# Kernel tuning notes

Hardware: AMD Instinct MI355X
Metric: run time of the kernel (lower is better)

Reference implementation:

```python
import jax, jax.numpy as jnp
import numpy as np
import math

B, S, H, NH = 8, 2048, 128, 4
DH = H // NH
SQRT_2_OVER_PI = math.sqrt(2.0 / math.pi)


def layer_norm(x, a, b, eps=1e-6):
    # Faithful to the torch module: unbiased std (ddof=1) and divide by (std + eps)
    mean = jnp.mean(x, axis=-1, keepdims=True)
    std = jnp.std(x, axis=-1, keepdims=True, ddof=1)
    return a * (x - mean) / (std + eps) + b


def setup_inputs() -> dict:
    key = jax.random.key(0)
    ks = jax.random.split(key, 10)
    inp = {
        "hidden": jax.random.normal(ks[0], (B, S, H), dtype=jnp.float32),
        "mask": jax.random.randint(ks[1], (B, S), 0, 2, dtype=jnp.int32),
        # attention params
        "attn_scale_w": jax.random.normal(ks[2], (NH, S), dtype=jnp.float32) * 0.1,
        "Wl": jax.random.normal(ks[3], (H, H), dtype=jnp.float32) * (1.0 / math.sqrt(H)),
        "bl": jnp.zeros((H,), dtype=jnp.float32),
        # FFN params
        "W1": jax.random.normal(ks[4], (H, H), dtype=jnp.float32) * (1.0 / math.sqrt(H)),
        "b1": jnp.zeros((H,), dtype=jnp.float32),
        "ffn_scale_w": jax.random.normal(ks[5], (S, 1), dtype=jnp.float32) * 0.1,
        # layer norms
        "ln1_a": jnp.ones((H,), dtype=jnp.float32),
        "ln1_b": jnp.zeros((H,), dtype=jnp.float32),
        "ln2_a": jnp.ones((H,), dtype=jnp.float32),
        "ln2_b": jnp.zeros((H,), dtype=jnp.float32),
    }
    return inp


def reference(hidden, mask, attn_scale_w, Wl, bl, W1, b1, ffn_scale_w,
              ln1_a, ln1_b, ln2_a, ln2_b):
    x = hidden  # [B, S, H]

    # --- attention sublayer (pre-norm residual) ---
    n1 = layer_norm(x, ln1_a, ln1_b)
    qkv = n1.reshape(B, S, NH, DH).transpose(0, 2, 1, 3)  # [B, NH, S, DH]
    # scores with per-head/per-query-position learned scale
    corr = jnp.einsum("bhqd,bhkd->bhqk", qkv, qkv) / math.sqrt(DH)
    corr = corr * attn_scale_w[None, :, :, None]  # scale over query positions
    # mask over key positions: [B,1,1,S], broadcast matches repeat in torch
    corr = jnp.where(mask[:, None, None, :] == 0, -1e9, corr)
    prob = jax.nn.softmax(corr, axis=-1)
    h = jnp.einsum("bhqk,bhkd->bhqd", prob, qkv)
    h = h.transpose(0, 2, 1, 3).reshape(B, S, H)
    attn_out = h @ Wl.T + bl
    x = x + attn_out

    # --- FFN sublayer (pre-norm residual) ---
    n2 = layer_norm(x, ln2_a, ln2_b)
    hf = ffn_scale_w[None] * (n2 @ W1.T + b1)  # [B, S, H] with per-position scale
    act = 0.5 * hf * (1.0 + jnp.tanh(SQRT_2_OVER_PI * (hf + 0.044715 * hf ** 3)))
    x = x + act

    return x
```

## Files before the change

### kernel.cpp

```cpp
#include <hip/hip_runtime.h>

#define BB 8
#define SS 2048
#define HH 128
#define NHH 4
#define DHH 32

typedef _Float16 f16;
typedef f16 f16x4 __attribute__((ext_vector_type(4)));
typedef f16 f16x8 __attribute__((ext_vector_type(8)));
typedef float f32x4 __attribute__((ext_vector_type(4)));

#define BIAS0 -5.7707801636f

__device__ __forceinline__ f16x8 cat(f16x4 a, f16x4 b) {
  return (f16x8){a[0], a[1], a[2], a[3], b[0], b[1], b[2], b[3]};
}

__device__ __forceinline__ f16x4 tr_read(const f16* p) {
  f16x4 d;
  asm volatile("ds_read_b64_tr_b16 %0, %1"
               : "=v"(d)
               : "v"((__attribute__((address_space(3))) const f16*)p)
               : "memory");
  return d;
}

__global__ __launch_bounds__(256) void stage1_kernel(const float* __restrict__ x,
                                                     const float* __restrict__ ga,
                                                     const float* __restrict__ gb,
                                                     const float* __restrict__ Wl,
                                                     const float* __restrict__ W1,
                                                     const int* __restrict__ mask,
                                                     f16* __restrict__ n1,
                                                     f16* __restrict__ Wlf,
                                                     f16* __restrict__ W1f,
                                                     int* __restrict__ idx,
                                                     int* __restrict__ nkcnt,
                                                     int* __restrict__ nkpad) {
  const int tid = threadIdx.x;
  if (blockIdx.x < 1024) {
    const int wave = tid >> 6, lane = tid & 63;
    const int grp = lane >> 4, lm = lane & 15;
    const int r = wave * 4 + grp;
    const size_t row = (size_t)blockIdx.x * 16 + r;

    const float* xr = x + row * HH + lm * 8;
    float4 v0 = *(const float4*)(xr);
    float4 v1 = *(const float4*)(xr + 4);
    float xv[8] = {v0.x, v0.y, v0.z, v0.w, v1.x, v1.y, v1.z, v1.w};
    float sum = 0.f, sq = 0.f;
#pragma unroll
    for (int j = 0; j < 8; ++j) { sum += xv[j]; sq += xv[j] * xv[j]; }
#pragma unroll
    for (int m = 1; m < 16; m <<= 1) {
      sum += __shfl_xor(sum, m);
      sq += __shfl_xor(sq, m);
    }
    float mean = sum * (1.0f / HH);
    float var = fmaxf((sq - (float)HH * mean * mean) * (1.0f / (HH - 1)), 0.0f);
    float inv = 1.0f / (sqrtf(var) + 1e-6f);

    float4 a0 = *(const float4*)(ga + lm * 8);
    float4 a1 = *(const float4*)(ga + lm * 8 + 4);
    float4 b0 = *(const float4*)(gb + lm * 8);
    float4 b1 = *(const float4*)(gb + lm * 8 + 4);
    float av[8] = {a0.x, a0.y, a0.z, a0.w, a1.x, a1.y, a1.z, a1.w};
    float bv[8] = {b0.x, b0.y, b0.z, b0.w, b1.x, b1.y, b1.z, b1.w};
    f16x8 w;
#pragma unroll
    for (int j = 0; j < 8; ++j) w[j] = (f16)(av[j] * (xv[j] - mean) * inv + bv[j]);
    *(f16x8*)(n1 + row * HH + lm * 8) = w;
    return;
  }
  if (blockIdx.x < 1056) {
    int g = (blockIdx.x - 1024) * 256 + tid;
    if (g < 4096) {
      float4 w = ((const float4*)Wl)[g];
      f16x4 o = {(f16)w.x, (f16)w.y, (f16)w.z, (f16)w.w};
      ((f16x4*)Wlf)[g] = o;
    } else {
      float4 w = ((const float4*)W1)[g - 4096];
      f16x4 o = {(f16)w.x, (f16)w.y, (f16)w.z, (f16)w.w};
      ((f16x4*)W1f)[g - 4096] = o;
    }
    return;
  }
  const int b = blockIdx.x - 1056;
  __shared__ int ps[256];
  int m8[8];
  int cnt = 0;
  const int* mp = mask + b * SS + tid * 8;
#pragma unroll
  for (int j = 0; j < 8; ++j) {
    m8[j] = mp[j];
    cnt += (m8[j] != 0);
  }
  ps[tid] = cnt;
  __syncthreads();
  for (int off = 1; off < 256; off <<= 1) {
    int v = (tid >= off) ? ps[tid - off] : 0;
    __syncthreads();
    ps[tid] += v;
    __syncthreads();
  }
  int pos = ps[tid] - cnt;
#pragma unroll
  for (int j = 0; j < 8; ++j) {
    if (m8[j] != 0) idx[b * SS + pos++] = tid * 8 + j;
  }
  __syncthreads();
  int nkv = ps[255];
  int npv = (nkv + 63) & ~63;
  if (npv == 0) npv = 64;
  for (int jj = nkv + tid; jj < npv; jj += 256) idx[b * SS + jj] = 0;
  if (tid == 255) { nkcnt[b] = nkv; nkpad[b] = npv; }
}

__global__ __launch_bounds__(256, 1) void attn_kernel(const f16* __restrict__ n1,
                                                      const int* __restrict__ idx,
                                                      const int* __restrict__ nkcnt,
                                                      const int* __restrict__ nkpad,
                                                      const float* __restrict__ scalew,
                                                      f16* __restrict__ hatt) {
  const int tid = threadIdx.x;
  const int qb = blockIdx.x & 7;
  const int h = (blockIdx.x >> 3) & 3;
  const int b = blockIdx.x >> 5;
  const int wave = tid >> 6, lane = tid & 63;
  const int lg = lane >> 4, lm = lane & 15;
  const int nk = nkcnt[b];
  const int ns = nkpad[b] >> 6;

  __shared__ __align__(16) f16 Kt[2][2][64][16];
  __shared__ __align__(16) int idxL[SS];

  const f16* __restrict__ nb = n1 + (size_t)b * SS * HH + h * DHH;

  const int np = ns << 6;
  for (int j = tid * 4; j < np; j += 1024)
    *(int4*)&idxL[j] = *(const int4*)(idx + b * SS + j);

  const int q0 = qb * 256 + wave * 64 + lm;
  f16x8 qf[4];
  float sc2[4];
#pragma unroll
  for (int qt = 0; qt < 4; ++qt) {
    int q = q0 + qt * 16;
    qf[qt] = *(const f16x8*)(nb + (size_t)q * HH + lg * 8);
    sc2[qt] = scalew[h * SS + q] * 0.2550680718664f;
  }

  const int sk = tid >> 2, sp = tid & 3;

  const f32x4 zero = {0.f, 0.f, 0.f, 0.f};
  f32x4 acc[4][2] = {{zero, zero}, {zero, zero}, {zero, zero}, {zero, zero}};
  f32x4 lacc[4] = {zero, zero, zero, zero};
  const f16x8 ones = {(f16)1, (f16)1, (f16)1, (f16)1, (f16)1, (f16)1, (f16)1, (f16)1};

  __syncthreads();
  {
    int row = idxL[sk];
    f16x8 kreg = *(const f16x8*)(nb + (size_t)row * HH + sp * 8);
    *(f16x8*)(&Kt[0][sp >> 1][sk][(sp & 1) * 8]) = kreg;
  }
  __syncthreads();

  for (int c = 0; c < ns; ++c) {
    const int buf = c & 1;
    const int k0 = c * 64;
    f16x8 kreg;
    if (c + 1 < ns) {
      int row = idxL[k0 + 64 + sk];
      kreg = *(const f16x8*)(nb + (size_t)row * HH + sp * 8);
    }
    f16x4 t0a = tr_read(&Kt[buf][0][0][0] + lane * 4);
    f16x4 t0b = tr_read(&Kt[buf][0][16][0] + lane * 4);
    f16x4 t0c = tr_read(&Kt[buf][0][32][0] + lane * 4);
    f16x4 t0d = tr_read(&Kt[buf][0][48][0] + lane * 4);
    f16x4 t1a = tr_read(&Kt[buf][1][0][0] + lane * 4);
    f16x4 t1b = tr_read(&Kt[buf][1][16][0] + lane * 4);
    f16x4 t1c = tr_read(&Kt[buf][1][32][0] + lane * 4);
    f16x4 t1d = tr_read(&Kt[buf][1][48][0] + lane * 4);

    f16x8 kf[4];
#pragma unroll
    for (int t = 0; t < 4; ++t)
      kf[t] = *(const f16x8*)(&Kt[buf][lg >> 1][t * 16 + lm][(lg & 1) * 8]);

    const bool tail = (k0 + 64 > nk);
    f16x8 pf[4][2];
#define PF_LOOP(MASKED)                                                                   \
  _Pragma("unroll") for (int qt = 0; qt < 4; ++qt) {                                      \
    _Pragma("unroll") for (int t = 0; t < 4; ++t) {                                       \
      f32x4 st = __builtin_amdgcn_mfma_f32_16x16x32_f16(kf[t], qf[qt], zero, 0, 0, 0);    \
      _Pragma("unroll") for (int r = 0; r < 4; ++r) {                                     \
        float pe = __builtin_amdgcn_exp2f(st[r] * sc2[qt] + BIAS0);                       \
        if (MASKED && (k0 + t * 16 + lg * 4 + r >= nk)) pe = 0.0f;                        \
        pf[qt][t >> 1][(t & 1) * 4 + r] = (f16)pe;                                        \
      }                                                                                   \
    }                                                                                     \
  }
    if (!tail) { PF_LOOP(false) } else { PF_LOOP(true) }
#undef PF_LOOP

#pragma unroll
    for (int qt = 0; qt < 4; ++qt) {
#pragma unroll
      for (int s = 0; s < 2; ++s)
        lacc[qt] = __builtin_amdgcn_mfma_f32_16x16x32_f16(ones, pf[qt][s], lacc[qt], 0, 0, 0);
    }

    asm volatile("s_waitcnt lgkmcnt(0)" ::: "memory");
    __builtin_amdgcn_sched_barrier(0);

    f16x8 vf;
    vf = cat(t0a, t0b);
#pragma unroll
    for (int qt = 0; qt < 4; ++qt)
      acc[qt][0] = __builtin_amdgcn_mfma_f32_16x16x32_f16(vf, pf[qt][0], acc[qt][0], 0, 0, 0);
    vf = cat(t1a, t1b);
#pragma unroll
    for (int qt = 0; qt < 4; ++qt)
      acc[qt][1] = __builtin_amdgcn_mfma_f32_16x16x32_f16(vf, pf[qt][0], acc[qt][1], 0, 0, 0);
    vf = cat(t0c, t0d);
#pragma unroll
    for (int qt = 0; qt < 4; ++qt)
      acc[qt][0] = __builtin_amdgcn_mfma_f32_16x16x32_f16(vf, pf[qt][1], acc[qt][0], 0, 0, 0);
    vf = cat(t1c, t1d);
#pragma unroll
    for (int qt = 0; qt < 4; ++qt)
      acc[qt][1] = __builtin_amdgcn_mfma_f32_16x16x32_f16(vf, pf[qt][1], acc[qt][1], 0, 0, 0);

    if (c + 1 < ns)
      *(f16x8*)(&Kt[buf ^ 1][sp >> 1][sk][(sp & 1) * 8]) = kreg;
    __syncthreads();
  }

#pragma unroll
  for (int qt = 0; qt < 4; ++qt) {
    float inv = 1.0f / lacc[qt][0];
    int q = q0 + qt * 16;
    f16* op = hatt + (size_t)(b * SS + q) * HH + h * DHH;
    f16x4 o0 = {(f16)(acc[qt][0][0] * inv), (f16)(acc[qt][0][1] * inv),
                (f16)(acc[qt][0][2] * inv), (f16)(acc[qt][0][3] * inv)};
    f16x4 o1 = {(f16)(acc[qt][1][0] * inv), (f16)(acc[qt][1][1] * inv),
                (f16)(acc[qt][1][2] * inv), (f16)(acc[qt][1][3] * inv)};
    *(f16x4*)(op + lg * 4) = o0;
    *(f16x4*)(op + 16 + lg * 4) = o1;
  }
}

__global__ __launch_bounds__(256) void mlp_kernel(const f16* __restrict__ X,
                                                  const f16* __restrict__ Wlf,
                                                  const float* __restrict__ bl,
                                                  const float* __restrict__ resid,
                                                  const float* __restrict__ ln2a,
                                                  const float* __restrict__ ln2b,
                                                  const f16* __restrict__ W1f,
                                                  const float* __restrict__ b1,
                                                  const float* __restrict__ fscale,
                                                  float* __restrict__ out) {
  const int tid = threadIdx.x;
  const int wave = tid >> 6, lane = tid & 63;
  const int lg = lane >> 4, lm = lane & 15;
  const int rbase = blockIdx.x * 32;
  const int nc0 = wave * 32;

  __shared__ __align__(16) f16 n2t[32][136];
  __shared__ float red[4][32][2];

  f32x4 acc[2][2] = {};
  const f16* xr0 = X + (size_t)(rbase + lm) * HH;
  const f16* xr1 = X + (size_t)(rbase + 16 + lm) * HH;
#pragma unroll
  for (int ks = 0; ks < 4; ++ks) {
    f16x8 bf0 = *(const f16x8*)(xr0 + ks * 32 + lg * 8);
    f16x8 bf1 = *(const f16x8*)(xr1 + ks * 32 + lg * 8);
#pragma unroll
    for (int nt = 0; nt < 2; ++nt) {
      f16x8 af = *(const f16x8*)(Wlf + (size_t)(nc0 + nt * 16 + lm) * HH + ks * 32 + lg * 8);
      acc[0][nt] = __builtin_amdgcn_mfma_f32_16x16x32_f16(af, bf0, acc[0][nt], 0, 0, 0);
      acc[1][nt] = __builtin_amdgcn_mfma_f32_16x16x32_f16(af, bf1, acc[1][nt], 0, 0, 0);
    }
  }
  float sum[2] = {0.f, 0.f}, sq[2] = {0.f, 0.f};
  f32x4 o[2][2];
#pragma unroll
  for (int g = 0; g < 2; ++g) {
    int row = rbase + g * 16 + lm;
#pragma unroll
    for (int nt = 0; nt < 2; ++nt) {
      int n = nc0 + nt * 16 + lg * 4;
      float4 rv = *(const float4*)(resid + (size_t)row * HH + n);
      float4 bv = *(const float4*)(bl + n);
      f32x4 v = acc[g][nt];
      v[0] += rv.x + bv.x; v[1] += rv.y + bv.y;
      v[2] += rv.z + bv.z; v[3] += rv.w + bv.w;
      o[g][nt] = v;
      sum[g] += v[0] + v[1] + v[2] + v[3];
      sq[g] += v[0] * v[0] + v[1] * v[1] + v[2] * v[2] + v[3] * v[3];
    }
    sum[g] += __shfl_xor(sum[g], 16); sum[g] += __shfl_xor(sum[g], 32);
    sq[g] += __shfl_xor(sq[g], 16);  sq[g] += __shfl_xor(sq[g], 32);
  }
  if (lane < 16) {
#pragma unroll
    for (int g = 0; g < 2; ++g) {
      red[wave][g * 16 + lm][0] = sum[g];
      red[wave][g * 16 + lm][1] = sq[g];
    }
  }
  __syncthreads();
#pragma unroll
  for (int g = 0; g < 2; ++g) {
    int lr = g * 16 + lm;
    float ts = red[0][lr][0] + red[1][lr][0] + red[2][lr][0] + red[3][lr][0];
    float tq = red[0][lr][1] + red[1][lr][1] + red[2][lr][1] + red[3][lr][1];
    float mean = ts * (1.0f / HH);
    float var = fmaxf((tq - (float)HH * mean * mean) * (1.0f / (HH - 1)), 0.0f);
    float inv = 1.0f / (sqrtf(var) + 1e-6f);
#pragma unroll
    for (int nt = 0; nt < 2; ++nt) {
      int n = nc0 + nt * 16 + lg * 4;
      float4 av = *(const float4*)(ln2a + n);
      float4 b2 = *(const float4*)(ln2b + n);
      f16x4 w;
      w[0] = (f16)(av.x * (o[g][nt][0] - mean) * inv + b2.x);
      w[1] = (f16)(av.y * (o[g][nt][1] - mean) * inv + b2.y);
      w[2] = (f16)(av.z * (o[g][nt][2] - mean) * inv + b2.z);
      w[3] = (f16)(av.w * (o[g][nt][3] - mean) * inv + b2.w);
      *(f16x4*)(&n2t[lr][n]) = w;
    }
  }
  __syncthreads();

  f32x4 fa[2][2] = {};
#pragma unroll
  for (int ks = 0; ks < 4; ++ks) {
    f16x8 bf0 = *(const f16x8*)(&n2t[lm][ks * 32 + lg * 8]);
    f16x8 bf1 = *(const f16x8*)(&n2t[16 + lm][ks * 32 + lg * 8]);
#pragma unroll
    for (int nt = 0; nt < 2; ++nt) {
      f16x8 af = *(const f16x8*)(W1f + (size_t)(nc0 + nt * 16 + lm) * HH + ks * 32 + lg * 8);
      fa[0][nt] = __builtin_amdgcn_mfma_f32_16x16x32_f16(af, bf0, fa[0][nt], 0, 0, 0);
      fa[1][nt] = __builtin_amdgcn_mfma_f32_16x16x32_f16(af, bf1, fa[1][nt], 0, 0, 0);
    }
  }
#pragma unroll
  for (int g = 0; g < 2; ++g) {
    int row = rbase + g * 16 + lm;
    float fs = fscale[row & (SS - 1)];
#pragma unroll
    for (int nt = 0; nt < 2; ++nt) {
      int n = nc0 + nt * 16 + lg * 4;
      float4 bv = *(const float4*)(b1 + n);
      const float* bp = &bv.x;
#pragma unroll
      for (int e = 0; e < 4; ++e) {
        float hf = fs * (fa[g][nt][e] + bp[e]);
        float u = 0.7978845608028654f * hf * (1.0f + 0.044715f * hf * hf);
        float ex = __builtin_amdgcn_exp2f(u * 2.8853900817779268f);
        float t = 1.0f - 2.0f / (ex + 1.0f);
        o[g][nt][e] += 0.5f * hf * (1.0f + t);
      }
      *(f32x4*)(out + (size_t)row * HH + n) = o[g][nt];
    }
  }
}

extern "C" void kernel_launch(void* const* d_in, const int* in_sizes, int n_in,
                              void* d_out, int out_size, void* d_ws, size_t ws_size,
                              hipStream_t stream) {
  const float* hidden = (const float*)d_in[0];
  const int* mask = (const int*)d_in[1];
  const float* scalew = (const float*)d_in[2];
  const float* Wl = (const float*)d_in[3];
  const float* bl = (const float*)d_in[4];
  const float* W1 = (const float*)d_in[5];
  const float* b1 = (const float*)d_in[6];
  const float* fscale = (const float*)d_in[7];
  const float* ln1a = (const float*)d_in[8];
  const float* ln1b = (const float*)d_in[9];
  const float* ln2a = (const float*)d_in[10];
  const float* ln2b = (const float*)d_in[11];
  float* out = (float*)d_out;

  const size_t NE = (size_t)BB * SS * HH;
  f16* n1 = (f16*)d_ws;
  f16* hattf = n1 + NE;
  f16* Wlf = hattf + NE;
  f16* W1f = Wlf + HH * HH;
  int* idx = (int*)(W1f + HH * HH);
  int* nkcnt = idx + BB * SS;
  int* nkpad = nkcnt + BB;

  stage1_kernel<<<1064, 256, 0, stream>>>(hidden, ln1a, ln1b, Wl, W1, mask,
                                          n1, Wlf, W1f, idx, nkcnt, nkpad);
  attn_kernel<<<BB * NHH * (SS / 256), 256, 0, stream>>>(n1, idx, nkcnt, nkpad,
                                                         scalew, hattf);
  mlp_kernel<<<BB * SS / 32, 256, 0, stream>>>(hattf, Wlf, bl, hidden, ln2a, ln2b,
                                               W1f, b1, fscale, out);
}
```

Before: 45.49 us.

## Split attention keys across waves with per-wave LDS tiles and cross-wave reduction

Each attention block now covers 64 queries instead of 256. Its four waves take disjoint strided key chunks, so the grid grows from 256 to 1024 blocks. Each wave owns a private double-use LDS K tile and prefetches its next chunk into registers, which removes the per-chunk block-wide __syncthreads. The partial numerators and denominators are then reduced through LDS into wave 0. This works because the softmax uses a fixed exponent bias with no running max. The cost is a larger LDS footprint, a final reduction step, and each wave re-reading the same query fragments.

```diff
diff --git a/kernel.cpp b/kernel.cpp
--- a/kernel.cpp
+++ b/kernel.cpp
@@ -124,24 +124,26 @@
                                                       const float* __restrict__ scalew,
                                                       f16* __restrict__ hatt) {
   const int tid = threadIdx.x;
-  const int qb = blockIdx.x & 7;
-  const int h = (blockIdx.x >> 3) & 3;
-  const int b = blockIdx.x >> 5;
+  const int qb = blockIdx.x & 31;
+  const int h = (blockIdx.x >> 5) & 3;
+  const int b = blockIdx.x >> 7;
   const int wave = tid >> 6, lane = tid & 63;
   const int lg = lane >> 4, lm = lane & 15;
   const int nk = nkcnt[b];
   const int ns = nkpad[b] >> 6;
 
-  __shared__ __align__(16) f16 Kt[2][2][64][16];
+  __shared__ __align__(16) f16 Kt[4][2][64][16];
   __shared__ __align__(16) int idxL[SS];
+  __shared__ float red[36][3][64];
 
   const f16* __restrict__ nb = n1 + (size_t)b * SS * HH + h * DHH;
+  f16* __restrict__ tile = &Kt[wave][0][0][0];
 
   const int np = ns << 6;
   for (int j = tid * 4; j < np; j += 1024)
     *(int4*)&idxL[j] = *(const int4*)(idx + b * SS + j);
 
-  const int q0 = qb * 256 + wave * 64 + lm;
+  const int q0 = qb * 64 + lm;
   f16x8 qf[4];
   float sc2[4];
 #pragma unroll
@@ -151,7 +153,8 @@
     sc2[qt] = scalew[h * SS + q] * 0.2550680718664f;
   }
 
-  const int sk = tid >> 2, sp = tid & 3;
+  const int skey = lane >> 1;
+  const int soff = (lane & 1) * 8;
 
   const f32x4 zero = {0.f, 0.f, 0.f, 0.f};
   f32x4 acc[4][2] = {{zero, zero}, {zero, zero}, {zero, zero}, {zero, zero}};
@@ -159,34 +162,43 @@
   const f16x8 ones = {(f16)1, (f16)1, (f16)1, (f16)1, (f16)1, (f16)1, (f16)1, (f16)1};
 
   __syncthreads();
-  {
-    int row = idxL[sk];
-    f16x8 kreg = *(const f16x8*)(nb + (size_t)row * HH + sp * 8);
-    *(f16x8*)(&Kt[0][sp >> 1][sk][(sp & 1) * 8]) = kreg;
-  }
-  __syncthreads();
-
-  for (int c = 0; c < ns; ++c) {
-    const int buf = c & 1;
+
+  if (wave < ns) {
+#pragma unroll
+    for (int i = 0; i < 4; ++i) {
+      int row = idxL[wave * 64 + (i & 1) * 32 + skey];
+      f16x8 v = *(const f16x8*)(nb + (size_t)row * HH + (i >> 1) * 16 + soff);
+      *(f16x8*)(tile + i * 512 + lane * 8) = v;
+    }
+  }
+
+  for (int c = wave; c < ns; c += 4) {
     const int k0 = c * 64;
-    f16x8 kreg;
-    if (c + 1 < ns) {
-      int row = idxL[k0 + 64 + sk];
-      kreg = *(const f16x8*)(nb + (size_t)row * HH + sp * 8);
-    }
-    f16x4 t0a = tr_read(&Kt[buf][0][0][0] + lane * 4);
-    f16x4 t0b = tr_read(&Kt[buf][0][16][0] + lane * 4);
-    f16x4 t0c = tr_read(&Kt[buf][0][32][0] + lane * 4);
-    f16x4 t0d = tr_read(&Kt[buf][0][48][0] + lane * 4);
-    f16x4 t1a = tr_read(&Kt[buf][1][0][0] + lane * 4);
-    f16x4 t1b = tr_read(&Kt[buf][1][16][0] + lane * 4);
-    f16x4 t1c = tr_read(&Kt[buf][1][32][0] + lane * 4);
-    f16x4 t1d = tr_read(&Kt[buf][1][48][0] + lane * 4);
+    f16x8 nreg[4];
+    const bool more = (c + 4 < ns);
+    if (more) {
+#pragma unroll
+      for (int i = 0; i < 4; ++i) {
+        int row = idxL[k0 + 256 + (i & 1) * 32 + skey];
+        nreg[i] = *(const f16x8*)(nb + (size_t)row * HH + (i >> 1) * 16 + soff);
+      }
+    }
+    f16x4 t0a = tr_read(tile + 0 * 512 + 0 + lane * 4);
+    f16x4 t0b = tr_read(tile + 0 * 512 + 256 + lane * 4);
+    f16x4 t0c = tr_read(tile + 1 * 512 + 0 + lane * 4);
+    f16x4 t0d = tr_read(tile + 1 * 512 + 256 + lane * 4);
+    f16x4 t1a = tr_read(tile + 2 * 512 + 0 + lane * 4);
+    f16x4 t1b = tr_read(tile + 2 * 512 + 256 + lane * 4);
+    f16x4 t1c = tr_read(tile + 3 * 512 + 0 + lane * 4);
+    f16x4 t1d = tr_read(tile + 3 * 512 + 256 + lane * 4);
 
     f16x8 kf[4];
 #pragma unroll
-    for (int t = 0; t < 4; ++t)
-      kf[t] = *(const f16x8*)(&Kt[buf][lg >> 1][t * 16 + lm][(lg & 1) * 8]);
+    for (int t = 0; t < 4; ++t) {
+      kf[t] = *(const f16x8*)(tile + (lg >> 1) * 1024 + (t >> 1) * 512 +
+                              ((t & 1) * 32 + lm - (t & 1) * 16 + ((t & 1) ? 16 : 0)) * 0 +
+                              (t & 1) * 0 + ((t * 16 + lm) & 31) * 16 + (lg & 1) * 8);
+    }
 
     const bool tail = (k0 + 64 > nk);
     f16x8 pf[4][2];
@@ -232,22 +244,50 @@
     for (int qt = 0; qt < 4; ++qt)
       acc[qt][1] = __builtin_amdgcn_mfma_f32_16x16x32_f16(vf, pf[qt][1], acc[qt][1], 0, 0, 0);
 
-    if (c + 1 < ns)
-      *(f16x8*)(&Kt[buf ^ 1][sp >> 1][sk][(sp & 1) * 8]) = kreg;
-    __syncthreads();
-  }
-
-#pragma unroll
-  for (int qt = 0; qt < 4; ++qt) {
-    float inv = 1.0f / lacc[qt][0];
-    int q = q0 + qt * 16;
-    f16* op = hatt + (size_t)(b * SS + q) * HH + h * DHH;
-    f16x4 o0 = {(f16)(acc[qt][0][0] * inv), (f16)(acc[qt][0][1] * inv),
-                (f16)(acc[qt][0][2] * inv), (f16)(acc[qt][0][3] * inv)};
-    f16x4 o1 = {(f16)(acc[qt][1][0] * inv), (f16)(acc[qt][1][1] * inv),
-                (f16)(acc[qt][1][2] * inv), (f16)(acc[qt][1][3] * inv)};
-    *(f16x4*)(op + lg * 4) = o0;
-    *(f16x4*)(op + 16 + lg * 4) = o1;
+    if (more) {
+#pragma unroll
+      for (int i = 0; i < 4; ++i)
+        *(f16x8*)(tile + i * 512 + lane * 8) = nreg[i];
+    }
+  }
+
+  if (wave > 0) {
+#pragma unroll
+    for (int qt = 0; qt < 4; ++qt) {
+#pragma unroll
+      for (int dh = 0; dh < 2; ++dh)
+#pragma unroll
+        for (int r = 0; r < 4; ++r)
+          red[qt * 8 + dh * 4 + r][wave - 1][lane] = acc[qt][dh][r];
+      red[32 + qt][wave - 1][lane] = lacc[qt][0];
+    }
+  }
+  __syncthreads();
+  if (wave == 0) {
+#pragma unroll
+    for (int w = 0; w < 3; ++w) {
+#pragma unroll
+      for (int qt = 0; qt < 4; ++qt) {
+#pragma unroll
+        for (int dh = 0; dh < 2; ++dh)
+#pragma unroll
+          for (int r = 0; r < 4; ++r)
+            acc[qt][dh][r] += red[qt * 8 + dh * 4 + r][w][lane];
+        lacc[qt][0] += red[32 + qt][w][lane];
+      }
+    }
+#pragma unroll
+    for (int qt = 0; qt < 4; ++qt) {
+      float inv = 1.0f / lacc[qt][0];
+      int q = q0 + qt * 16;
+      f16* op = hatt + (size_t)(b * SS + q) * HH + h * DHH;
+      f16x4 o0 = {(f16)(acc[qt][0][0] * inv), (f16)(acc[qt][0][1] * inv),
+                  (f16)(acc[qt][0][2] * inv), (f16)(acc[qt][0][3] * inv)};
+      f16x4 o1 = {(f16)(acc[qt][1][0] * inv), (f16)(acc[qt][1][1] * inv),
+                  (f16)(acc[qt][1][2] * inv), (f16)(acc[qt][1][3] * inv)};
+      *(f16x4*)(op + lg * 4) = o0;
+      *(f16x4*)(op + 16 + lg * 4) = o1;
+    }
   }
 }
 
@@ -397,8 +437,8 @@
 
   stage1_kernel<<<1064, 256, 0, stream>>>(hidden, ln1a, ln1b, Wl, W1, mask,
                                           n1, Wlf, W1f, idx, nkcnt, nkpad);
-  attn_kernel<<<BB * NHH * (SS / 256), 256, 0, stream>>>(n1, idx, nkcnt, nkpad,
-                                                         scalew, hattf);
+  attn_kernel<<<BB * NHH * (SS / 64), 256, 0, stream>>>(n1, idx, nkcnt, nkpad,
+                                                        scalew, hattf);
   mlp_kernel<<<BB * SS / 32, 256, 0, stream>>>(hattf, Wlf, bl, hidden, ln2a, ln2b,
                                                W1f, b1, fscale, out);
 }
```

New measurement: 48.06 us. 1.06x slower.
